# Performance work log

Hardware: AMD Instinct MI355X
Metric: run time of the kernel (lower is better)

The kernel has to match this reference:

```python
import jax, jax.numpy as jnp
import numpy as np

N_NODES = 100000


def gcn_conv(x, W, b, src, dst, n):
    # PyG GCNConv: linear transform, add self-loops, symmetric deg^-1/2 norm,
    # scatter-sum messages from src -> dst, add bias.
    x = x @ W  # [N, out]
    loop = jnp.arange(n, dtype=src.dtype)
    src_sl = jnp.concatenate([src, loop])
    dst_sl = jnp.concatenate([dst, loop])
    deg = jax.ops.segment_sum(jnp.ones_like(dst_sl, dtype=x.dtype), dst_sl, num_segments=n)
    dinv = jax.lax.rsqrt(deg)
    norm = dinv[src_sl] * dinv[dst_sl]  # [E+N]
    msg = x[src_sl] * norm[:, None]
    out = jax.ops.segment_sum(msg, dst_sl, num_segments=n)
    return out + b


def base_gnn(x, edge_index, W1, b1, W2, b2):
    src, dst = edge_index[0], edge_index[1]
    n = x.shape[0]
    h = gcn_conv(x, W1, b1, src, dst, n)
    h = jax.nn.relu(h)
    return gcn_conv(h, W2, b2, src, dst, n)


def setup_inputs() -> dict:
    key = jax.random.key(0)
    ks = jax.random.split(key, 12)
    n, e, ep, en = N_NODES, 1600000, 200000, 200000
    in_ch, hid, out_ch, n_classes = 256, 128, 128, 10
    x = jax.random.normal(ks[0], (n, in_ch), dtype=jnp.float32)
    edge_index = jax.random.randint(ks[1], (2, e), 0, n, dtype=jnp.int64)
    edge_index_pos = jax.random.randint(ks[2], (2, ep), 0, n, dtype=jnp.int64)
    edge_index_neg = jax.random.randint(ks[3], (2, en), 0, n, dtype=jnp.int64)
    s1 = 1.0 / np.sqrt(in_ch)
    s2 = 1.0 / np.sqrt(hid)
    so = 1.0 / np.sqrt(out_ch)
    sl = 1.0 / np.sqrt(2 * out_ch)
    return {
        "x": x,
        "edge_index": edge_index,
        "edge_index_pos": edge_index_pos,
        "edge_index_neg": edge_index_neg,
        "W1": jax.random.uniform(ks[4], (in_ch, hid), jnp.float32, -s1, s1),
        "b1": jnp.zeros((hid,), jnp.float32),
        "W2": jax.random.uniform(ks[5], (hid, out_ch), jnp.float32, -s2, s2),
        "b2": jnp.zeros((out_ch,), jnp.float32),
        "Wcls": jax.random.uniform(ks[6], (out_ch, n_classes), jnp.float32, -so, so),
        "bcls": jax.random.uniform(ks[7], (n_classes,), jnp.float32, -so, so),
        "Wlink": jax.random.uniform(ks[8], (2 * out_ch, 1), jnp.float32, -sl, sl),
        "blink": jax.random.uniform(ks[9], (1,), jnp.float32, -sl, sl),
    }


def reference(x, edge_index, edge_index_pos, edge_index_neg,
              W1, b1, W2, b2, Wcls, bcls, Wlink, blink):
    # Shared base embedding (math identical to torch's redundant recompute)
    h = base_gnn(x, edge_index, W1, b1, W2, b2)  # [N, 128]
    # Node head
    node_logits = jax.nn.relu(h) @ Wcls + bcls
    node_pred = jax.nn.log_softmax(node_logits, axis=1)
    # Link head: gather endpoint embeddings, concat, linear
    xp = jnp.concatenate([h[edge_index_pos[0]], h[edge_index_pos[1]]], axis=1)
    xn = jnp.concatenate([h[edge_index_neg[0]], h[edge_index_neg[1]]], axis=1)
    link_pos = (xp @ Wlink + blink)[:, 0]
    link_neg = (xn @ Wlink + blink)[:, 0]
    return (node_pred, link_pos, link_neg)
```

## Files before the change

### kernel.cpp

```cpp
#include <hip/hip_runtime.h>
#include <stdint.h>

typedef __attribute__((ext_vector_type(8))) short bf16x8;
typedef __attribute__((ext_vector_type(4))) float f32x4;

__device__ __forceinline__ float b2f(uint32_t h) {
    union { uint32_t u; float f; } v; v.u = h << 16; return v.f;
}
__device__ __forceinline__ ushort f2b(float f) {
    union { float f; uint32_t u; } v; v.f = f;
    uint32_t u = v.u;
    return (ushort)((u + 0x7fffu + ((u >> 16) & 1u)) >> 16);
}
__device__ __forceinline__ float ldin(const void* p, int i, int fp32) {
    return fp32 ? ((const float*)p)[i] : b2f(((const ushort*)p)[i]);
}

__device__ __forceinline__ void sniff(const void* W1, const void* ei, int* sf) {
    if (threadIdx.x < 64) {
        int l = threadIdx.x;
        const ushort* w = (const ushort*)W1;
        bool bad = !(fabsf(b2f(w[l])) <= 0.25f) || !(fabsf(b2f(w[64 + l])) <= 0.25f);
        unsigned long long mb = __ballot(bad);
        const int* e = (const int*)ei;
        bool z = (l < 16) ? (e[2 * l + 1] == 0) : false;
        unsigned long long mz = __ballot(z);
        if (l == 0) {
            sf[0] = mb ? 1 : 0;
            sf[1] = (__popcll(mz & 0xffffull) >= 15) ? 1 : 0;
        }
    }
    __syncthreads();
}


__global__ __launch_bounds__(256) void k_prep(const void* __restrict__ x,
                                              const void* ei, const void* ep, const void* en,
                                              const void* W1, const void* b1, const void* W2,
                                              const void* b2, const void* Wc, const void* bc,
                                              const void* Wl, const void* bl,
                                              int* cEi, int* cEp, int* cEn,
                                              ushort* __restrict__ xc,
                                              ushort* Wt1, ushort* Wt2, ushort* WtC,
                                              ushort* b1c, ushort* b2c, ushort* bcc,
                                              ushort* Wlc, ushort* blc,
                                              int* __restrict__ histM,
                                              int twoEp, int twoEn, int N,
                                              int E, int NB1,
                                              int Bidx, int Bw, int Bx) {
    __shared__ int sf[2];
    __shared__ int h[512];
    sniff(W1, ei, sf);
    int f = sf[0], i64 = sf[1];
    int b = blockIdx.x;

    if (b < Bidx) {
        int i = (b * 256 + threadIdx.x) * 2;
        const void* srcp; int* dstp; int j = i;
        if (i < E) { srcp = ei; dstp = cEi; }
        else if (i < E + twoEp) { srcp = ep; dstp = cEp; j = i - E; }
        else if (i < E + twoEp + twoEn) { srcp = en; dstp = cEn; j = i - E - twoEp; }
        else return;
        int v0, v1;
        if (i64) {
            longlong2 t = *(const longlong2*)((const long long*)srcp + j);
            v0 = (int)t.x; v1 = (int)t.y;
        } else {
            int2 t = *(const int2*)((const int*)srcp + j);
            v0 = t.x; v1 = t.y;
        }
        v0 = v0 < 0 ? 0 : (v0 >= N ? N - 1 : v0);
        v1 = v1 < 0 ? 0 : (v1 >= N ? N - 1 : v1);
        *(int2*)(dstp + j) = make_int2(v0, v1);
    } else if (b < Bidx + Bw) {
        int i = (b - Bidx) * 256 + threadIdx.x;
        if (i < 32768) {
            int c = i >> 8, kpos = i & 255;
            int s = kpos >> 5, t = kpos & 31, q = t >> 3, jj = t & 7;
            int k = s * 32 + (jj < 4 ? q * 4 + jj : 16 + q * 4 + (jj - 4));
            Wt1[i] = f2b(ldin(W1, k * 128 + c, f));
        } else if (i < 49152) {
            int j = i - 32768, c = j >> 7, k = j & 127;
            Wt2[j] = f2b(ldin(W2, k * 128 + c, f));
        } else if (i < 51200) {
            int j = i - 49152, c = j >> 7, k = j & 127;
            ushort v = 0;
            if (c < 10) v = f2b(ldin(Wc, k * 10 + c, f));
            WtC[j] = v;
        } else if (i < 51328) {
            int j = i - 51200; b1c[j] = f2b(ldin(b1, j, f));
        } else if (i < 51456) {
            int j = i - 51328; b2c[j] = f2b(ldin(b2, j, f));
        } else if (i < 51472) {
            int j = i - 51456;
            ushort v = 0;
            if (j < 10) v = f2b(ldin(bc, j, f));
            bcc[j] = v;
        } else if (i < 51728) {
            int j = i - 51472; Wlc[j] = f2b(ldin(Wl, j, f));
        } else if (i < 51736) {
            int j = i - 51728;
            ushort v = 0;
            if (j < 1) v = f2b(ldin(bl, 0, f));
            blc[j] = v;
        }
    } else if (b < Bidx + Bw + Bx) {
        int gw = (b - Bidx - Bw) * 4 + (threadIdx.x >> 6);
        int ntile = (N + 15) >> 4;
        if (gw >= ntile * 4) return;
        int tile = gw >> 2, s2 = gw & 3;
        int l = threadIdx.x & 63, mr = l & 15, q = l >> 4;
        int row = tile * 16 + mr;
        if (row > N - 1) row = N - 1;
#pragma unroll
        for (int u = 0; u < 2; ++u) {
            int s = s2 * 2 + u;
            uint4 o;
            if (f) {
                const float* xf = (const float*)x + (size_t)row * 256 + s * 32;
                float4 a = *(const float4*)(xf + q * 4);
                float4 bb = *(const float4*)(xf + 16 + q * 4);
                o.x = (uint32_t)f2b(a.x) | ((uint32_t)f2b(a.y) << 16);
                o.y = (uint32_t)f2b(a.z) | ((uint32_t)f2b(a.w) << 16);
                o.z = (uint32_t)f2b(bb.x) | ((uint32_t)f2b(bb.y) << 16);
                o.w = (uint32_t)f2b(bb.z) | ((uint32_t)f2b(bb.w) << 16);
            } else {
                const ushort* xs = (const ushort*)x + (size_t)row * 256 + s * 32;
                uint2 lo = *(const uint2*)(xs + q * 4);
                uint2 hi = *(const uint2*)(xs + 16 + q * 4);
                o.x = lo.x; o.y = lo.y; o.z = hi.x; o.w = hi.y;
            }
            *(uint4*)(xc + ((size_t)(tile * 8 + s) * 64 + l) * 8) = o;
        }
    } else {
        int b2 = b - Bidx - Bw - Bx;
        for (int j = threadIdx.x; j < 512; j += 256) h[j] = 0;
        __syncthreads();
        int base = b2 * 4096;
        for (int j = threadIdx.x; j < 4096; j += 256) {
            int i = base + j;
            if (i < E) {
                int d = i64 ? (int)((const long long*)ei)[E + i] : ((const int*)ei)[E + i];
                d = d < 0 ? 0 : (d >= N ? N - 1 : d);
                cEi[E + i] = d;
                atomicAdd(&h[d >> 8], 1);
            }
        }
        __syncthreads();
        for (int j = threadIdx.x; j < 512; j += 256)
            histM[j * NB1 + b2] = h[j];
    }
}

__global__ __launch_bounds__(1024) void k_mscan_block(const int* __restrict__ in, int* __restrict__ out,
                                                      int* __restrict__ bsum, int len) {
    __shared__ int sh[1024];
    int t = threadIdx.x;
    int i = blockIdx.x * 1024 + t;
    int val = (i < len) ? in[i] : 0;
    sh[t] = val; __syncthreads();
    for (int off = 1; off < 1024; off <<= 1) {
        int v = (t >= off) ? sh[t - off] : 0;
        __syncthreads();
        sh[t] += v;
        __syncthreads();
    }
    if (i < len) out[i] = sh[t] - val;
    if (t == 1023) bsum[blockIdx.x] = sh[1023];
}

__global__ __launch_bounds__(1024) void k_mscan_topadd(int* __restrict__ out, const int* __restrict__ bsum,
                                                       int* __restrict__ cbs, int len, int mb,
                                                       int NB1, int E) {
    __shared__ int sh[1024];
    int t = threadIdx.x;
    sh[t] = (t < mb) ? bsum[t] : 0; __syncthreads();
    for (int off = 1; off < 1024; off <<= 1) {
        int v = (t >= off) ? sh[t - off] : 0;
        __syncthreads();
        sh[t] += v;
        __syncthreads();
    }
    int pref = (blockIdx.x > 0) ? sh[blockIdx.x - 1] : 0;
    int i = blockIdx.x * 1024 + t;
    if (i < len) {
        int v = out[i] + pref;
        out[i] = v;
        if (i % NB1 == 0) cbs[i / NB1] = v;
    }
    if (i == 0) cbs[512] = E;
}

__global__ __launch_bounds__(256) void k_scatter1(const int* __restrict__ src, const int* __restrict__ dst,
                                                  const int* __restrict__ off, int2* __restrict__ grouped,
                                                  int E, int NB1) {
    __shared__ int o[512];
    for (int j = threadIdx.x; j < 512; j += 256) o[j] = off[j * NB1 + blockIdx.x];
    __syncthreads();
    int base = blockIdx.x * 4096;
    for (int j = threadIdx.x; j < 4096; j += 256) {
        int i = base + j;
        if (i < E) {
            int d = dst[i];
            int p = atomicAdd(&o[d >> 8], 1);
            grouped[p] = make_int2(src[i], d);
        }
    }
}

__global__ __launch_bounds__(256) void k_degfill(const int2* __restrict__ grouped, const int* __restrict__ cbs,
                                                 int* __restrict__ rowptr, float* __restrict__ dinv,
                                                 int* __restrict__ edgeS, int N, int E) {
    __shared__ int cnt[256];
    __shared__ int obase[256];
    int t = threadIdx.x, b = blockIdx.x;
    cnt[t] = 0;
    __syncthreads();
    int s0 = cbs[b], s1 = cbs[b + 1];
    for (int i = s0 + t; i < s1; i += 256)
        atomicAdd(&cnt[grouped[i].y & 255], 1);
    __syncthreads();
    int deg = cnt[t];
    __syncthreads();
    for (int off = 1; off < 256; off <<= 1) {
        int vv = (t >= off) ? cnt[t - off] : 0;
        __syncthreads();
        cnt[t] += vv;
        __syncthreads();
    }
    int excl = cnt[t] - deg;
    int v = b * 256 + t;
    if (v < N) {
        rowptr[v] = s0 + excl;
        dinv[v] = rsqrtf((float)(deg + 1));
    }
    if (b == 0 && t == 0) rowptr[N] = E;
    obase[t] = s0 + excl;
    __syncthreads();
    for (int i = s0 + t; i < s1; i += 256) {
        int2 e = grouped[i];
        int p = atomicAdd(&obase[e.y & 255], 1);
        edgeS[p] = e.x;
    }
}

template <int NS>
__global__ __launch_bounds__(256) void k_gemm(const ushort* __restrict__ Xf,
                                              const ushort* __restrict__ Wt,
                                              ushort* __restrict__ Out, int nrows) {
    __shared__ uint4 sB[NS * 8 * 64];

    const int tid = threadIdx.x;
    for (int it = tid; it < NS * 8 * 64; it += 256) {
        int l = it & 63, fn = it >> 6;
        int s = fn >> 3, n = fn & 7;
        int mr = l & 15, q = l >> 4;
        sB[it] = *(const uint4*)(Wt + (size_t)(n * 16 + mr) * (NS * 32) + s * 32 + q * 8);
    }
    __syncthreads();

    const int wave = tid >> 6;
    const int l = tid & 63;
    const int q = l >> 4, mr = l & 15;
    const int gw = blockIdx.x * 4 + wave;
    const int nw = gridDim.x * 4;
    const int ntile = (nrows + 15) >> 4;

    for (int tp = gw; tp * 4 < ntile; tp += nw) {
        const int t0 = tp * 4;
        const bool h1 = (t0 + 1 < ntile), h2 = (t0 + 2 < ntile), h3 = (t0 + 3 < ntile);
        const int tb1 = h1 ? t0 + 1 : t0, tb2 = h2 ? t0 + 2 : t0, tb3 = h3 ? t0 + 3 : t0;

        const ushort* x0 = Xf + ((size_t)t0 * NS * 64 + l) * 8;
        const ushort* x1 = Xf + ((size_t)tb1 * NS * 64 + l) * 8;
        const ushort* x2 = Xf + ((size_t)tb2 * NS * 64 + l) * 8;
        const ushort* x3 = Xf + ((size_t)tb3 * NS * 64 + l) * 8;

        f32x4 accA[8], accB[8], accC[8], accD[8];
#pragma unroll
        for (int n = 0; n < 8; ++n) {
            accA[n] = (f32x4){0.f, 0.f, 0.f, 0.f};
            accB[n] = (f32x4){0.f, 0.f, 0.f, 0.f};
            accC[n] = (f32x4){0.f, 0.f, 0.f, 0.f};
            accD[n] = (f32x4){0.f, 0.f, 0.f, 0.f};
        }
#pragma unroll
        for (int s = 0; s < NS; ++s) {
            bf16x8 a0 = *(const bf16x8*)(x0 + s * 512);
            bf16x8 a1 = *(const bf16x8*)(x1 + s * 512);
            bf16x8 a2 = *(const bf16x8*)(x2 + s * 512);
            bf16x8 a3 = *(const bf16x8*)(x3 + s * 512);
#pragma unroll
            for (int n = 0; n < 8; ++n) {
                bf16x8 bfr = __builtin_bit_cast(bf16x8, sB[(s * 8 + n) * 64 + l]);
                accA[n] = __builtin_amdgcn_mfma_f32_16x16x32_bf16(bfr, a0, accA[n], 0, 0, 0);
                accB[n] = __builtin_amdgcn_mfma_f32_16x16x32_bf16(bfr, a1, accB[n], 0, 0, 0);
                accC[n] = __builtin_amdgcn_mfma_f32_16x16x32_bf16(bfr, a2, accC[n], 0, 0, 0);
                accD[n] = __builtin_amdgcn_mfma_f32_16x16x32_bf16(bfr, a3, accD[n], 0, 0, 0);
            }
        }
        {
            int row = t0 * 16 + mr;
            if (row < nrows) {
                ushort* orow = Out + (size_t)row * 128 + q * 4;
#pragma unroll
                for (int n = 0; n < 8; ++n) {
                    uint2 o;
                    o.x = (uint32_t)f2b(accA[n][0]) | ((uint32_t)f2b(accA[n][1]) << 16);
                    o.y = (uint32_t)f2b(accA[n][2]) | ((uint32_t)f2b(accA[n][3]) << 16);
                    *(uint2*)(orow + n * 16) = o;
                }
            }
        }
        if (h1) {
            int row = tb1 * 16 + mr;
            if (row < nrows) {
                ushort* orow = Out + (size_t)row * 128 + q * 4;
#pragma unroll
                for (int n = 0; n < 8; ++n) {
                    uint2 o;
                    o.x = (uint32_t)f2b(accB[n][0]) | ((uint32_t)f2b(accB[n][1]) << 16);
                    o.y = (uint32_t)f2b(accB[n][2]) | ((uint32_t)f2b(accB[n][3]) << 16);
                    *(uint2*)(orow + n * 16) = o;
                }
            }
        }
        if (h2) {
            int row = tb2 * 16 + mr;
            if (row < nrows) {
                ushort* orow = Out + (size_t)row * 128 + q * 4;
#pragma unroll
                for (int n = 0; n < 8; ++n) {
                    uint2 o;
                    o.x = (uint32_t)f2b(accC[n][0]) | ((uint32_t)f2b(accC[n][1]) << 16);
                    o.y = (uint32_t)f2b(accC[n][2]) | ((uint32_t)f2b(accC[n][3]) << 16);
                    *(uint2*)(orow + n * 16) = o;
                }
            }
        }
        if (h3) {
            int row = tb3 * 16 + mr;
            if (row < nrows) {
                ushort* orow = Out + (size_t)row * 128 + q * 4;
#pragma unroll
                for (int n = 0; n < 8; ++n) {
                    uint2 o;
                    o.x = (uint32_t)f2b(accD[n][0]) | ((uint32_t)f2b(accD[n][1]) << 16);
                    o.y = (uint32_t)f2b(accD[n][2]) | ((uint32_t)f2b(accD[n][3]) << 16);
                    *(uint2*)(orow + n * 16) = o;
                }
            }
        }
    }
}

__device__ __forceinline__ void fma8(float* acc, uint4 p, float w) {
    uint32_t pu[4] = {p.x, p.y, p.z, p.w};
#pragma unroll
    for (int k = 0; k < 4; ++k) {
        float lo = __uint_as_float(pu[k] << 16);
        float hi = __uint_as_float(pu[k] & 0xffff0000u);
        acc[2 * k]     += lo * w;
        acc[2 * k + 1] += hi * w;
    }
}

__global__ __launch_bounds__(256) void k_conv(const ushort* __restrict__ XW, const int* __restrict__ rowptr,
                                              const int* __restrict__ edgeS, const float* __restrict__ dinv,
                                              const ushort* __restrict__ bias, ushort* __restrict__ Hout,
                                              int n, int relu, int frag) {
    int wave = threadIdx.x >> 6;
    int v = blockIdx.x * 4 + wave;
    if (v >= n) return;
    int l = threadIdx.x & 63;
    int g = l >> 4;
    int c = l & 15;

    int s0 = rowptr[v], s1 = rowptr[v + 1];
    float dv = dinv[v];
    float wself = (g == 0) ? dv * dv : 0.f;

    uint4 pv = *(const uint4*)(XW + (size_t)v * 128 + c * 8);
    float acc[8];
    {
        uint32_t pu[4] = {pv.x, pv.y, pv.z, pv.w};
#pragma unroll
        for (int k = 0; k < 4; ++k) {
            acc[2 * k]     = __uint_as_float(pu[k] << 16) * wself;
            acc[2 * k + 1] = __uint_as_float(pu[k] & 0xffff0000u) * wself;
        }
    }

    int i = s0;
    while (i + 16 <= s1) {
        int sA = edgeS[i + g];
        int sB = edgeS[i + 4 + g];
        int sC = edgeS[i + 8 + g];
        int sD = edgeS[i + 12 + g];
        uint4 pA = *(const uint4*)(XW + (size_t)sA * 128 + c * 8);
        uint4 pB = *(const uint4*)(XW + (size_t)sB * 128 + c * 8);
        uint4 pC = *(const uint4*)(XW + (size_t)sC * 128 + c * 8);
        uint4 pD = *(const uint4*)(XW + (size_t)sD * 128 + c * 8);
        float wA = dinv[sA] * dv, wB = dinv[sB] * dv;
        float wC = dinv[sC] * dv, wD = dinv[sD] * dv;
        fma8(acc, pA, wA);
        fma8(acc, pB, wB);
        fma8(acc, pC, wC);
        fma8(acc, pD, wD);
        i += 16;
    }
    if (i + 8 <= s1) {
        int sA = edgeS[i + g];
        int sB = edgeS[i + 4 + g];
        uint4 pA = *(const uint4*)(XW + (size_t)sA * 128 + c * 8);
        uint4 pB = *(const uint4*)(XW + (size_t)sB * 128 + c * 8);
        float wA = dinv[sA] * dv, wB = dinv[sB] * dv;
        fma8(acc, pA, wA);
        fma8(acc, pB, wB);
        i += 8;
    }
    if (i + 4 <= s1) {
        int sA = edgeS[i + g];
        uint4 pA = *(const uint4*)(XW + (size_t)sA * 128 + c * 8);
        fma8(acc, pA, dinv[sA] * dv);
        i += 4;
    }
    if (i < s1) {
        int ei_ = i + g;
        bool val = ei_ < s1;
        int sA = edgeS[val ? ei_ : s0];
        uint4 pA = *(const uint4*)(XW + (size_t)sA * 128 + c * 8);
        fma8(acc, pA, val ? dinv[sA] * dv : 0.f);
    }

#pragma unroll
    for (int k = 0; k < 8; ++k) {
        acc[k] += __shfl_xor(acc[k], 16);
        acc[k] += __shfl_xor(acc[k], 32);
    }

    if (g == 0) {
        uint4 bb = *(const uint4*)(bias + c * 8);
        uint32_t bu[4] = {bb.x, bb.y, bb.z, bb.w};
        uint4 o;
        uint32_t* op = (uint32_t*)&o;
#pragma unroll
        for (int k = 0; k < 4; ++k) {
            float lo = acc[2 * k]     + __uint_as_float(bu[k] << 16);
            float hi = acc[2 * k + 1] + __uint_as_float(bu[k] & 0xffff0000u);
            if (relu) { lo = fmaxf(lo, 0.f); hi = fmaxf(hi, 0.f); }
            op[k] = (uint32_t)f2b(lo) | ((uint32_t)f2b(hi) << 16);
        }
        if (frag) {
            int tile = v >> 4, mr = v & 15;
            size_t chunk = ((size_t)(tile * 4 + (c >> 2)) * 64 + (c & 3) * 16 + mr);
            *(uint4*)(Hout + chunk * 8) = o;
        } else {
            *(uint4*)(Hout + (size_t)v * 128 + c * 8) = o;
        }
    }
}

__global__ __launch_bounds__(256) void k_nodehead(const ushort* __restrict__ H, const ushort* __restrict__ WtC,
                                                  const ushort* __restrict__ bcc, const ushort* __restrict__ Wlc,
                                                  float2* __restrict__ ab, void* __restrict__ out,
                                                  int n, const void* W1s, const void* eis) {
    __shared__ int sf[2];
    sniff(W1s, eis, sf);
    int fp32o = sf[0];
    int wave = threadIdx.x >> 6;
    int gw = blockIdx.x * 4 + wave;
    if (gw * 16 >= n) return;
    int l = threadIdx.x & 63;
    int q = l >> 4, mr = l & 15;
    int m0 = gw * 16;

    const ushort* hrow = H + (size_t)(m0 + mr) * 128 + q * 8;
    bf16x8 araw[4];
#pragma unroll
    for (int s = 0; s < 4; ++s) araw[s] = *(const bf16x8*)(hrow + s * 32);

    float pa = 0.f, pb = 0.f;
#pragma unroll
    for (int s = 0; s < 4; ++s) {
        bf16x8 w0 = *(const bf16x8*)(Wlc + s * 32 + q * 8);
        bf16x8 w1 = *(const bf16x8*)(Wlc + 128 + s * 32 + q * 8);
#pragma unroll
        for (int j = 0; j < 8; ++j) {
            float hv = b2f((ushort)araw[s][j]);
            pa += hv * b2f((ushort)w0[j]);
            pb += hv * b2f((ushort)w1[j]);
        }
    }
    pa += __shfl_xor(pa, 16); pa += __shfl_xor(pa, 32);
    pb += __shfl_xor(pb, 16); pb += __shfl_xor(pb, 32);
    if (q == 0 && (m0 + mr) < n) ab[m0 + mr] = make_float2(pa, pb);

    f32x4 acc = (f32x4){0.f, 0.f, 0.f, 0.f};
#pragma unroll
    for (int s = 0; s < 4; ++s) {
        bf16x8 a = araw[s];
#pragma unroll
        for (int j = 0; j < 8; ++j) {
            ushort t = (ushort)a[j];
            if (t & 0x8000u) a[j] = 0;
        }
        bf16x8 b = *(const bf16x8*)(WtC + (size_t)mr * 128 + s * 32 + q * 8);
        acc = __builtin_amdgcn_mfma_f32_16x16x32_bf16(a, b, acc, 0, 0, 0);
    }

    float bc = b2f(bcc[mr]);
#pragma unroll
    for (int r = 0; r < 4; ++r) {
        float logit = acc[r] + bc;
        float m = (mr < 10) ? logit : -1e30f;
#pragma unroll
        for (int off = 1; off < 16; off <<= 1) m = fmaxf(m, __shfl_xor(m, off, 16));
        float ex = (mr < 10) ? expf(logit - m) : 0.f;
        float ssum = ex;
#pragma unroll
        for (int off = 1; off < 16; off <<= 1) ssum += __shfl_xor(ssum, off, 16);
        int row = m0 + q * 4 + r;
        if (mr < 10 && row < n) {
            float lsm = logit - m - logf(ssum);
            size_t idx = (size_t)row * 10 + mr;
            if (fp32o) ((float*)out)[idx] = lsm;
            else ((ushort*)out)[idx] = f2b(lsm);
        }
    }
}

__global__ __launch_bounds__(256) void k_linkfast(const float2* __restrict__ ab, const int* __restrict__ pos,
                                                  const int* __restrict__ neg, const ushort* __restrict__ blc,
                                                  void* __restrict__ out, size_t obase, int Ep, int En,
                                                  const void* W1s, const void* eis) {
    __shared__ int sf[2];
    sniff(W1s, eis, sf);
    int i = blockIdx.x * 256 + threadIdx.x;
    if (i >= Ep + En) return;
    int s, d;
    if (i < Ep) { s = pos[i]; d = pos[Ep + i]; }
    else { int j = i - Ep; s = neg[j]; d = neg[En + j]; }
    float vf = ab[s].x + ab[d].y + b2f(blc[0]);
    size_t idx = obase + (size_t)i;
    if (sf[0]) ((float*)out)[idx] = vf;
    else ((ushort*)out)[idx] = f2b(vf);
}

extern "C" void kernel_launch(void* const* d_in, const int* in_sizes, int n_in,
                              void* d_out, int out_size, void* d_ws, size_t ws_size,
                              hipStream_t stream) {
    const void* x    = d_in[0];
    const void* ei   = d_in[1];
    const void* eip  = d_in[2];
    const void* ein  = d_in[3];
    const void* W1   = d_in[4];
    const void* b1   = d_in[5];
    const void* W2   = d_in[6];
    const void* b2   = d_in[7];
    const void* Wcls = d_in[8];
    const void* bcls = d_in[9];
    const void* Wl   = d_in[10];
    const void* bl   = d_in[11];

    const int N  = in_sizes[0] / 256;
    const int E  = in_sizes[1] / 2;
    const int Ep = in_sizes[2] / 2;
    const int En = in_sizes[3] / 2;

    const int NB1  = (E + 4095) / 4096;
    const int mlen = 512 * NB1;
    const int mb   = (mlen + 1023) / 1024;
    const int ntile = (N + 15) / 16;

    char* ws = (char*)d_ws;
    size_t off = 0;
    auto alloc = [&](size_t bytes) -> void* {
        void* p = ws + off;
        off = (off + bytes + 255) & ~(size_t)255;
        return p;
    };
    ushort* xc     = (ushort*)alloc((size_t)ntile * 8 * 64 * 16);
    ushort* bufXW  = (ushort*)alloc((size_t)N * 128 * 2);
    ushort* bufH   = (ushort*)alloc((size_t)ntile * 4 * 64 * 16);
    float2* ab     = (float2*)alloc((size_t)N * 8);
    int*    cEi    = (int*)alloc((size_t)2 * E * 4);
    int*    cEp    = (int*)alloc((size_t)2 * Ep * 4);
    int*    cEn    = (int*)alloc((size_t)2 * En * 4);
    int2*   grouped= (int2*)alloc((size_t)E * 8);
    int*    histM  = (int*)alloc((size_t)mlen * 4);
    int*    offM   = (int*)alloc((size_t)mlen * 4);
    int*    msum   = (int*)alloc(4096);
    int*    cbs    = (int*)alloc(513 * 4);
    float*  dinv   = (float*)alloc((size_t)N * 4);
    int*    rowp   = (int*)alloc((size_t)(N + 1) * 4);
    int*    edgeS  = (int*)alloc((size_t)E * 4);
    ushort* Wt1    = (ushort*)alloc(65536);
    ushort* Wt2    = (ushort*)alloc(32768);
    ushort* WtC    = (ushort*)alloc(4096);
    ushort* b1c    = (ushort*)alloc(256);
    ushort* b2c    = (ushort*)alloc(256);
    ushort* bcc    = (ushort*)alloc(64);
    ushort* Wlc    = (ushort*)alloc(512);
    ushort* blc    = (ushort*)alloc(64);

    int twoEp = 2 * Ep, twoEn = 2 * En;
    int idx_total = E + twoEp + twoEn;
    int Bidx = (idx_total + 511) / 512;
    int Bw   = 203;
    int Bx   = ntile;

    k_prep<<<Bidx + Bw + Bx + NB1, 256, 0, stream>>>(x, ei, eip, ein, W1, b1, W2, b2, Wcls, bcls, Wl, bl,
                                                     cEi, cEp, cEn, xc, Wt1, Wt2, WtC,
                                                     b1c, b2c, bcc, Wlc, blc, histM,
                                                     twoEp, twoEn, N, E, NB1,
                                                     Bidx, Bw, Bx);

    const int* srcp = cEi;
    const int* dstp = cEi + E;

    k_mscan_block<<<mb, 1024, 0, stream>>>(histM, offM, msum, mlen);
    k_mscan_topadd<<<mb, 1024, 0, stream>>>(offM, msum, cbs, mlen, mb, NB1, E);
    k_scatter1<<<NB1, 256, 0, stream>>>(srcp, dstp, offM, grouped, E, NB1);
    k_degfill<<<512, 256, 0, stream>>>(grouped, cbs, rowp, dinv, edgeS, N, E);

    int quads = (ntile + 3) / 4;
    int g1 = (quads + 3) / 4; if (g1 > 768) g1 = 768;
    k_gemm<8><<<g1, 256, 0, stream>>>(xc, Wt1, bufXW, N);
    k_conv<<<(N + 3) / 4, 256, 0, stream>>>(bufXW, rowp, edgeS, dinv, b1c, bufH, N, 1, 1);
    k_gemm<4><<<g1, 256, 0, stream>>>(bufH, Wt2, bufXW, N);
    k_conv<<<(N + 3) / 4, 256, 0, stream>>>(bufXW, rowp, edgeS, dinv, b2c, bufH, N, 0, 0);

    int head_blocks = ((N + 15) / 16 + 3) / 4;
    k_nodehead<<<head_blocks, 256, 0, stream>>>(bufH, WtC, bcc, Wlc, ab, d_out, N, W1, ei);
    k_linkfast<<<(Ep + En + 255) / 256, 256, 0, stream>>>(ab, cEp, cEn, blc, d_out,
                                                          (size_t)N * 10, Ep, En, W1, ei);
}
```

Before: 444.7 us.

## Fuse fp32-to-bf16 conversion of x into first GEMM A-operand loads

Removes the separate pass in the prep kernel that converted x to bf16 and wrote it in an MFMA-friendly tiled layout. The first GEMM now reads raw x rows directly (fp32 or bf16, detected by the sniff routine) and converts to bf16 in registers before the MFMA. This drops one full write and re-read of the converted x buffer (about 51MB of traffic). The cost is less coalesced strided row loads, conversion work inside the GEMM, and a sniff call added to every GEMM block, including the second GEMM where it is not needed.

Result: no change. 447.4 us (+0.6%).

```diff
diff --git a/kernel.cpp b/kernel.cpp
--- a/kernel.cpp
+++ b/kernel.cpp
@@ -34,20 +34,18 @@
 }
 
 
-__global__ __launch_bounds__(256) void k_prep(const void* __restrict__ x,
-                                              const void* ei, const void* ep, const void* en,
+__global__ __launch_bounds__(256) void k_prep(const void* ei, const void* ep, const void* en,
                                               const void* W1, const void* b1, const void* W2,
                                               const void* b2, const void* Wc, const void* bc,
                                               const void* Wl, const void* bl,
                                               int* cEi, int* cEp, int* cEn,
-                                              ushort* __restrict__ xc,
                                               ushort* Wt1, ushort* Wt2, ushort* WtC,
                                               ushort* b1c, ushort* b2c, ushort* bcc,
                                               ushort* Wlc, ushort* blc,
                                               int* __restrict__ histM,
                                               int twoEp, int twoEn, int N,
                                               int E, int NB1,
-                                              int Bidx, int Bw, int Bx) {
+                                              int Bidx, int Bw) {
     __shared__ int sf[2];
     __shared__ int h[512];
     sniff(W1, ei, sf);
@@ -104,36 +102,8 @@
             if (j < 1) v = f2b(ldin(bl, 0, f));
             blc[j] = v;
         }
-    } else if (b < Bidx + Bw + Bx) {
-        int gw = (b - Bidx - Bw) * 4 + (threadIdx.x >> 6);
-        int ntile = (N + 15) >> 4;
-        if (gw >= ntile * 4) return;
-        int tile = gw >> 2, s2 = gw & 3;
-        int l = threadIdx.x & 63, mr = l & 15, q = l >> 4;
-        int row = tile * 16 + mr;
-        if (row > N - 1) row = N - 1;
-#pragma unroll
-        for (int u = 0; u < 2; ++u) {
-            int s = s2 * 2 + u;
-            uint4 o;
-            if (f) {
-                const float* xf = (const float*)x + (size_t)row * 256 + s * 32;
-                float4 a = *(const float4*)(xf + q * 4);
-                float4 bb = *(const float4*)(xf + 16 + q * 4);
-                o.x = (uint32_t)f2b(a.x) | ((uint32_t)f2b(a.y) << 16);
-                o.y = (uint32_t)f2b(a.z) | ((uint32_t)f2b(a.w) << 16);
-                o.z = (uint32_t)f2b(bb.x) | ((uint32_t)f2b(bb.y) << 16);
-                o.w = (uint32_t)f2b(bb.z) | ((uint32_t)f2b(bb.w) << 16);
-            } else {
-                const ushort* xs = (const ushort*)x + (size_t)row * 256 + s * 32;
-                uint2 lo = *(const uint2*)(xs + q * 4);
-                uint2 hi = *(const uint2*)(xs + 16 + q * 4);
-                o.x = lo.x; o.y = lo.y; o.z = hi.x; o.w = hi.y;
-            }
-            *(uint4*)(xc + ((size_t)(tile * 8 + s) * 64 + l) * 8) = o;
-        }
     } else {
-        int b2 = b - Bidx - Bw - Bx;
+        int b2 = b - Bidx - Bw;
         for (int j = threadIdx.x; j < 512; j += 256) h[j] = 0;
         __syncthreads();
         int base = b2 * 4096;
@@ -244,12 +214,16 @@
     }
 }
 
-template <int NS>
-__global__ __launch_bounds__(256) void k_gemm(const ushort* __restrict__ Xf,
+template <int NS, bool FUSE>
+__global__ __launch_bounds__(256) void k_gemm(const void* __restrict__ Xraw,
                                               const ushort* __restrict__ Wt,
-                                              ushort* __restrict__ Out, int nrows) {
+                                              ushort* __restrict__ Out, int nrows,
+                                              const void* W1s, const void* eis) {
+    __shared__ int sf[2];
+    sniff(W1s, eis, sf);
+    const bool f32in = FUSE && sf[0];
+
     __shared__ uint4 sB[NS * 8 * 64];
-
     const int tid = threadIdx.x;
     for (int it = tid; it < NS * 8 * 64; it += 256) {
         int l = it & 63, fn = it >> 6;
@@ -265,16 +239,17 @@
     const int gw = blockIdx.x * 4 + wave;
     const int nw = gridDim.x * 4;
     const int ntile = (nrows + 15) >> 4;
+    const int K = NS * 32;
 
     for (int tp = gw; tp * 4 < ntile; tp += nw) {
         const int t0 = tp * 4;
         const bool h1 = (t0 + 1 < ntile), h2 = (t0 + 2 < ntile), h3 = (t0 + 3 < ntile);
         const int tb1 = h1 ? t0 + 1 : t0, tb2 = h2 ? t0 + 2 : t0, tb3 = h3 ? t0 + 3 : t0;
 
-        const ushort* x0 = Xf + ((size_t)t0 * NS * 64 + l) * 8;
-        const ushort* x1 = Xf + ((size_t)tb1 * NS * 64 + l) * 8;
-        const ushort* x2 = Xf + ((size_t)tb2 * NS * 64 + l) * 8;
-        const ushort* x3 = Xf + ((size_t)tb3 * NS * 64 + l) * 8;
+        int r0 = t0 * 16 + mr;  if (r0 > nrows - 1) r0 = nrows - 1;
+        int r1 = tb1 * 16 + mr; if (r1 > nrows - 1) r1 = nrows - 1;
+        int r2 = tb2 * 16 + mr; if (r2 > nrows - 1) r2 = nrows - 1;
+        int r3 = tb3 * 16 + mr; if (r3 > nrows - 1) r3 = nrows - 1;
 
         f32x4 accA[8], accB[8], accC[8], accD[8];
 #pragma unroll
@@ -286,10 +261,44 @@
         }
 #pragma unroll
         for (int s = 0; s < NS; ++s) {
-            bf16x8 a0 = *(const bf16x8*)(x0 + s * 512);
-            bf16x8 a1 = *(const bf16x8*)(x1 + s * 512);
-            bf16x8 a2 = *(const bf16x8*)(x2 + s * 512);
-            bf16x8 a3 = *(const bf16x8*)(x3 + s * 512);
+            bf16x8 a0, a1, a2, a3;
+            if (FUSE) {
+                if (f32in) {
+                    const float* x0 = (const float*)Xraw + (size_t)r0 * K + s * 32;
+                    const float* x1 = (const float*)Xraw + (size_t)r1 * K + s * 32;
+                    const float* x2 = (const float*)Xraw + (size_t)r2 * K + s * 32;
+                    const float* x3 = (const float*)Xraw + (size_t)r3 * K + s * 32;
+                    float4 lo, hi;
+#define LOADCVT(dst, xp)                                                        \
+                    lo = *(const float4*)((xp) + q * 4);                        \
+                    hi = *(const float4*)((xp) + 16 + q * 4);                   \
+                    dst[0] = (short)f2b(lo.x); dst[1] = (short)f2b(lo.y);       \
+                    dst[2] = (short)f2b(lo.z); dst[3] = (short)f2b(lo.w);       \
+                    dst[4] = (short)f2b(hi.x); dst[5] = (short)f2b(hi.y);       \
+                    dst[6] = (short)f2b(hi.z); dst[7] = (short)f2b(hi.w);
+                    LOADCVT(a0, x0) LOADCVT(a1, x1) LOADCVT(a2, x2) LOADCVT(a3, x3)
+#undef LOADCVT
+                } else {
+                    const ushort* x0 = (const ushort*)Xraw + (size_t)r0 * K + s * 32;
+                    const ushort* x1 = (const ushort*)Xraw + (size_t)r1 * K + s * 32;
+                    const ushort* x2 = (const ushort*)Xraw + (size_t)r2 * K + s * 32;
+                    const ushort* x3 = (const ushort*)Xraw + (size_t)r3 * K + s * 32;
+                    uint2 lo, hi; uint4 m;
+#define LOADB(dst, xp)                                                          \
+                    lo = *(const uint2*)((xp) + q * 4);                         \
+                    hi = *(const uint2*)((xp) + 16 + q * 4);                    \
+                    m = (uint4){lo.x, lo.y, hi.x, hi.y};                        \
+                    dst = __builtin_bit_cast(bf16x8, m);
+                    LOADB(a0, x0) LOADB(a1, x1) LOADB(a2, x2) LOADB(a3, x3)
+#undef LOADB
+                }
+            } else {
+                const ushort* Xf = (const ushort*)Xraw;
+                a0 = *(const bf16x8*)(Xf + ((size_t)t0 * NS * 64 + l) * 8 + s * 512);
+                a1 = *(const bf16x8*)(Xf + ((size_t)tb1 * NS * 64 + l) * 8 + s * 512);
+                a2 = *(const bf16x8*)(Xf + ((size_t)tb2 * NS * 64 + l) * 8 + s * 512);
+                a3 = *(const bf16x8*)(Xf + ((size_t)tb3 * NS * 64 + l) * 8 + s * 512);
+            }
 #pragma unroll
             for (int n = 0; n < 8; ++n) {
                 bf16x8 bfr = __builtin_bit_cast(bf16x8, sB[(s * 8 + n) * 64 + l]);
@@ -580,7 +589,6 @@
         off = (off + bytes + 255) & ~(size_t)255;
         return p;
     };
-    ushort* xc     = (ushort*)alloc((size_t)ntile * 8 * 64 * 16);
     ushort* bufXW  = (ushort*)alloc((size_t)N * 128 * 2);
     ushort* bufH   = (ushort*)alloc((size_t)ntile * 4 * 64 * 16);
     float2* ab     = (float2*)alloc((size_t)N * 8);
@@ -608,13 +616,12 @@
     int idx_total = E + twoEp + twoEn;
     int Bidx = (idx_total + 511) / 512;
     int Bw   = 203;
-    int Bx   = ntile;
-
-    k_prep<<<Bidx + Bw + Bx + NB1, 256, 0, stream>>>(x, ei, eip, ein, W1, b1, W2, b2, Wcls, bcls, Wl, bl,
-                                                     cEi, cEp, cEn, xc, Wt1, Wt2, WtC,
-                                                     b1c, b2c, bcc, Wlc, blc, histM,
-                                                     twoEp, twoEn, N, E, NB1,
-                                                     Bidx, Bw, Bx);
+
+    k_prep<<<Bidx + Bw + NB1, 256, 0, stream>>>(ei, eip, ein, W1, b1, W2, b2, Wcls, bcls, Wl, bl,
+                                                cEi, cEp, cEn, Wt1, Wt2, WtC,
+                                                b1c, b2c, bcc, Wlc, blc, histM,
+                                                twoEp, twoEn, N, E, NB1,
+                                                Bidx, Bw);
 
     const int* srcp = cEi;
     const int* dstp = cEi + E;
@@ -626,9 +633,9 @@
 
     int quads = (ntile + 3) / 4;
     int g1 = (quads + 3) / 4; if (g1 > 768) g1 = 768;
-    k_gemm<8><<<g1, 256, 0, stream>>>(xc, Wt1, bufXW, N);
+    k_gemm<8, true><<<g1, 256, 0, stream>>>(x, Wt1, bufXW, N, W1, ei);
     k_conv<<<(N + 3) / 4, 256, 0, stream>>>(bufXW, rowp, edgeS, dinv, b1c, bufH, N, 1, 1);
-    k_gemm<4><<<g1, 256, 0, stream>>>(bufH, Wt2, bufXW, N);
+    k_gemm<4, false><<<g1, 256, 0, stream>>>(bufH, Wt2, bufXW, N, W1, ei);
     k_conv<<<(N + 3) / 4, 256, 0, stream>>>(bufXW, rowp, edgeS, dinv, b2c, bufH, N, 0, 0);
 
     int head_blocks = ((N + 15) / 16 + 3) / 4;
```

## Fuse fp32-to-bf16 conversion of x into first-layer GEMM kernel

Applied to the files above, without the earlier changes.

Drops the separate pass in k_prep that converted x to bf16 and laid it out in MFMA fragment order in a workspace buffer. The new k_gemm1 reads raw x rows directly, packs them to bf16 in registers, and computes two 16-row tiles per wave iteration with a fixed 512-block grid. This removes a full write and re-read of the converted x (about 51MB) in exchange for less coalesced strided loads inside the GEMM and higher register pressure.

Result: slower. 473.0 us (+6.4%).

```diff
diff --git a/kernel.cpp b/kernel.cpp
--- a/kernel.cpp
+++ b/kernel.cpp
@@ -14,6 +14,14 @@
 }
 __device__ __forceinline__ float ldin(const void* p, int i, int fp32) {
     return fp32 ? ((const float*)p)[i] : b2f(((const ushort*)p)[i]);
+}
+__device__ __forceinline__ bf16x8 pack8(float4 a, float4 b) {
+    bf16x8 r;
+    r[0] = (short)f2b(a.x); r[1] = (short)f2b(a.y);
+    r[2] = (short)f2b(a.z); r[3] = (short)f2b(a.w);
+    r[4] = (short)f2b(b.x); r[5] = (short)f2b(b.y);
+    r[6] = (short)f2b(b.z); r[7] = (short)f2b(b.w);
+    return r;
 }
 
 __device__ __forceinline__ void sniff(const void* W1, const void* ei, int* sf) {
@@ -34,20 +42,18 @@
 }
 
 
-__global__ __launch_bounds__(256) void k_prep(const void* __restrict__ x,
-                                              const void* ei, const void* ep, const void* en,
+__global__ __launch_bounds__(256) void k_prep(const void* ei, const void* ep, const void* en,
                                               const void* W1, const void* b1, const void* W2,
                                               const void* b2, const void* Wc, const void* bc,
                                               const void* Wl, const void* bl,
                                               int* cEi, int* cEp, int* cEn,
-                                              ushort* __restrict__ xc,
                                               ushort* Wt1, ushort* Wt2, ushort* WtC,
                                               ushort* b1c, ushort* b2c, ushort* bcc,
                                               ushort* Wlc, ushort* blc,
                                               int* __restrict__ histM,
                                               int twoEp, int twoEn, int N,
                                               int E, int NB1,
-                                              int Bidx, int Bw, int Bx) {
+                                              int Bidx, int Bw) {
     __shared__ int sf[2];
     __shared__ int h[512];
     sniff(W1, ei, sf);
@@ -104,36 +110,8 @@
             if (j < 1) v = f2b(ldin(bl, 0, f));
             blc[j] = v;
         }
-    } else if (b < Bidx + Bw + Bx) {
-        int gw = (b - Bidx - Bw) * 4 + (threadIdx.x >> 6);
-        int ntile = (N + 15) >> 4;
-        if (gw >= ntile * 4) return;
-        int tile = gw >> 2, s2 = gw & 3;
-        int l = threadIdx.x & 63, mr = l & 15, q = l >> 4;
-        int row = tile * 16 + mr;
-        if (row > N - 1) row = N - 1;
-#pragma unroll
-        for (int u = 0; u < 2; ++u) {
-            int s = s2 * 2 + u;
-            uint4 o;
-            if (f) {
-                const float* xf = (const float*)x + (size_t)row * 256 + s * 32;
-                float4 a = *(const float4*)(xf + q * 4);
-                float4 bb = *(const float4*)(xf + 16 + q * 4);
-                o.x = (uint32_t)f2b(a.x) | ((uint32_t)f2b(a.y) << 16);
-                o.y = (uint32_t)f2b(a.z) | ((uint32_t)f2b(a.w) << 16);
-                o.z = (uint32_t)f2b(bb.x) | ((uint32_t)f2b(bb.y) << 16);
-                o.w = (uint32_t)f2b(bb.z) | ((uint32_t)f2b(bb.w) << 16);
-            } else {
-                const ushort* xs = (const ushort*)x + (size_t)row * 256 + s * 32;
-                uint2 lo = *(const uint2*)(xs + q * 4);
-                uint2 hi = *(const uint2*)(xs + 16 + q * 4);
-                o.x = lo.x; o.y = lo.y; o.z = hi.x; o.w = hi.y;
-            }
-            *(uint4*)(xc + ((size_t)(tile * 8 + s) * 64 + l) * 8) = o;
-        }
     } else {
-        int b2 = b - Bidx - Bw - Bx;
+        int b2 = b - Bidx - Bw;
         for (int j = threadIdx.x; j < 512; j += 256) h[j] = 0;
         __syncthreads();
         int base = b2 * 4096;
@@ -244,10 +222,121 @@
     }
 }
 
+__global__ __launch_bounds__(256, 2) void k_gemm1(const void* __restrict__ Xraw,
+                                                  const ushort* __restrict__ Wt,
+                                                  ushort* __restrict__ Out, int nrows,
+                                                  const void* W1s, const void* eis) {
+    __shared__ int sf[2];
+    sniff(W1s, eis, sf);
+    const bool f32in = sf[0] != 0;
+
+    __shared__ uint4 sB[8 * 8 * 64];
+    const int tid = threadIdx.x;
+    for (int it = tid; it < 8 * 8 * 64; it += 256) {
+        int l = it & 63, fn = it >> 6;
+        int s = fn >> 3, n = fn & 7;
+        int mr = l & 15, q = l >> 4;
+        sB[it] = *(const uint4*)(Wt + (size_t)(n * 16 + mr) * 256 + s * 32 + q * 8);
+    }
+    __syncthreads();
+
+    const int wave = tid >> 6;
+    const int l = tid & 63;
+    const int q = l >> 4, mr = l & 15;
+    const int gw = blockIdx.x * 4 + wave;
+    const int nw = gridDim.x * 4;
+    const int ntile = (nrows + 15) >> 4;
+
+    for (int tp = gw; tp * 2 < ntile; tp += nw) {
+        const int t0 = tp * 2;
+        const bool has1 = (t0 + 1 < ntile);
+        const int t1 = has1 ? t0 + 1 : t0;
+        const int r0 = min(t0 * 16 + mr, nrows - 1);
+        const int r1 = min(t1 * 16 + mr, nrows - 1);
+
+        bf16x8 a0[8], a1[8];
+        if (f32in) {
+            const float* x0 = (const float*)Xraw + (size_t)r0 * 256;
+            const float* x1 = (const float*)Xraw + (size_t)r1 * 256;
+#pragma unroll
+            for (int s = 0; s < 8; ++s) {
+                float4 lo = *(const float4*)(x0 + s * 32 + q * 4);
+                float4 hi = *(const float4*)(x0 + s * 32 + 16 + q * 4);
+                a0[s] = pack8(lo, hi);
+            }
+#pragma unroll
+            for (int s = 0; s < 8; ++s) {
+                float4 lo = *(const float4*)(x1 + s * 32 + q * 4);
+                float4 hi = *(const float4*)(x1 + s * 32 + 16 + q * 4);
+                a1[s] = pack8(lo, hi);
+            }
+        } else {
+            const ushort* x0 = (const ushort*)Xraw + (size_t)r0 * 256;
+            const ushort* x1 = (const ushort*)Xraw + (size_t)r1 * 256;
+#pragma unroll
+            for (int s = 0; s < 8; ++s) {
+                uint2 lo = *(const uint2*)(x0 + s * 32 + q * 4);
+                uint2 hi = *(const uint2*)(x0 + s * 32 + 16 + q * 4);
+                uint4 m = (uint4){lo.x, lo.y, hi.x, hi.y};
+                a0[s] = __builtin_bit_cast(bf16x8, m);
+            }
+#pragma unroll
+            for (int s = 0; s < 8; ++s) {
+                uint2 lo = *(const uint2*)(x1 + s * 32 + q * 4);
+                uint2 hi = *(const uint2*)(x1 + s * 32 + 16 + q * 4);
+                uint4 m = (uint4){lo.x, lo.y, hi.x, hi.y};
+                a1[s] = __builtin_bit_cast(bf16x8, m);
+            }
+        }
+
+        f32x4 acc0[8], acc1[8];
+#pragma unroll
+        for (int n = 0; n < 8; ++n) {
+            acc0[n] = (f32x4){0.f, 0.f, 0.f, 0.f};
+            acc1[n] = (f32x4){0.f, 0.f, 0.f, 0.f};
+        }
+#pragma unroll
+        for (int s = 0; s < 8; ++s) {
+#pragma unroll
+            for (int n = 0; n < 8; ++n) {
+                bf16x8 bfr = __builtin_bit_cast(bf16x8, sB[(s * 8 + n) * 64 + l]);
+                acc0[n] = __builtin_amdgcn_mfma_f32_16x16x32_bf16(bfr, a0[s], acc0[n], 0, 0, 0);
+                acc1[n] = __builtin_amdgcn_mfma_f32_16x16x32_bf16(bfr, a1[s], acc1[n], 0, 0, 0);
+            }
+        }
+        {
+            int row = t0 * 16 + mr;
+            if (row < nrows) {
+                ushort* orow = Out + (size_t)row * 128 + q * 4;
+#pragma unroll
+                for (int n = 0; n < 8; ++n) {
+                    uint2 o;
+                    o.x = (uint32_t)f2b(acc0[n][0]) | ((uint32_t)f2b(acc0[n][1]) << 16);
+                    o.y = (uint32_t)f2b(acc0[n][2]) | ((uint32_t)f2b(acc0[n][3]) << 16);
+                    *(uint2*)(orow + n * 16) = o;
+                }
+            }
+        }
+        if (has1) {
+            int row = t1 * 16 + mr;
+            if (row < nrows) {
+                ushort* orow = Out + (size_t)row * 128 + q * 4;
+#pragma unroll
+                for (int n = 0; n < 8; ++n) {
+                    uint2 o;
+                    o.x = (uint32_t)f2b(acc1[n][0]) | ((uint32_t)f2b(acc1[n][1]) << 16);
+                    o.y = (uint32_t)f2b(acc1[n][2]) | ((uint32_t)f2b(acc1[n][3]) << 16);
+                    *(uint2*)(orow + n * 16) = o;
+                }
+            }
+        }
+    }
+}
+
 template <int NS>
-__global__ __launch_bounds__(256) void k_gemm(const ushort* __restrict__ Xf,
-                                              const ushort* __restrict__ Wt,
-                                              ushort* __restrict__ Out, int nrows) {
+__global__ __launch_bounds__(256) void k_gemm2(const ushort* __restrict__ Xf,
+                                               const ushort* __restrict__ Wt,
+                                               ushort* __restrict__ Out, int nrows) {
     __shared__ uint4 sB[NS * 8 * 64];
 
     const int tid = threadIdx.x;
@@ -580,7 +669,6 @@
         off = (off + bytes + 255) & ~(size_t)255;
         return p;
     };
-    ushort* xc     = (ushort*)alloc((size_t)ntile * 8 * 64 * 16);
     ushort* bufXW  = (ushort*)alloc((size_t)N * 128 * 2);
     ushort* bufH   = (ushort*)alloc((size_t)ntile * 4 * 64 * 16);
     float2* ab     = (float2*)alloc((size_t)N * 8);
@@ -608,13 +696,12 @@
     int idx_total = E + twoEp + twoEn;
     int Bidx = (idx_total + 511) / 512;
     int Bw   = 203;
-    int Bx   = ntile;
-
-    k_prep<<<Bidx + Bw + Bx + NB1, 256, 0, stream>>>(x, ei, eip, ein, W1, b1, W2, b2, Wcls, bcls, Wl, bl,
-                                                     cEi, cEp, cEn, xc, Wt1, Wt2, WtC,
-                                                     b1c, b2c, bcc, Wlc, blc, histM,
-                                                     twoEp, twoEn, N, E, NB1,
-                                                     Bidx, Bw, Bx);
+
+    k_prep<<<Bidx + Bw + NB1, 256, 0, stream>>>(ei, eip, ein, W1, b1, W2, b2, Wcls, bcls, Wl, bl,
+                                                cEi, cEp, cEn, Wt1, Wt2, WtC,
+                                                b1c, b2c, bcc, Wlc, blc, histM,
+                                                twoEp, twoEn, N, E, NB1,
+                                                Bidx, Bw);
 
     const int* srcp = cEi;
     const int* dstp = cEi + E;
@@ -624,11 +711,11 @@
     k_scatter1<<<NB1, 256, 0, stream>>>(srcp, dstp, offM, grouped, E, NB1);
     k_degfill<<<512, 256, 0, stream>>>(grouped, cbs, rowp, dinv, edgeS, N, E);
 
+    k_gemm1<<<512, 256, 0, stream>>>(x, Wt1, bufXW, N, W1, ei);
+    k_conv<<<(N + 3) / 4, 256, 0, stream>>>(bufXW, rowp, edgeS, dinv, b1c, bufH, N, 1, 1);
     int quads = (ntile + 3) / 4;
-    int g1 = (quads + 3) / 4; if (g1 > 768) g1 = 768;
-    k_gemm<8><<<g1, 256, 0, stream>>>(xc, Wt1, bufXW, N);
-    k_conv<<<(N + 3) / 4, 256, 0, stream>>>(bufXW, rowp, edgeS, dinv, b1c, bufH, N, 1, 1);
-    k_gemm<4><<<g1, 256, 0, stream>>>(bufH, Wt2, bufXW, N);
+    int g2 = (quads + 3) / 4; if (g2 > 768) g2 = 768;
+    k_gemm2<4><<<g2, 256, 0, stream>>>(bufH, Wt2, bufXW, N);
     k_conv<<<(N + 3) / 4, 256, 0, stream>>>(bufXW, rowp, edgeS, dinv, b2c, bufH, N, 0, 0);
 
     int head_blocks = ((N + 15) / 16 + 3) / 4;
```
